# Optimization experiments

Hardware: AMD Instinct MI355X
Metric: run time of the kernel (lower is better)

Reference implementation:

```python
import jax, jax.numpy as jnp
import numpy as np

RC = 5.0
P = 6
N_ATOM = 4
N_AXIS = 8
EPS = 1e-5
C_RES = 0.89442719  # sqrt(0.8)
C_NEW = 0.4472      # ~sqrt(0.2)
BESSEL_PREF = float(np.sqrt(2.0 / RC))


def poly_cutoff(x):
    # nequip-style PolynomialCutoff, p=6
    xr = x / RC
    p = float(P)
    out = (1.0
           - (p + 1.0) * (p + 2.0) / 2.0 * xr ** P
           + p * (p + 2.0) * xr ** (P + 1)
           - p * (p + 1.0) / 2.0 * xr ** (P + 2))
    return jnp.where(xr < 1.0, out, 0.0)


def bessel(x, w):
    # x: [E], w: [n_basis] (trainable n*pi weights)
    return BESSEL_PREF * jnp.sin(w * x[:, None] / RC) / x[:, None]


def layer_norm(x, g, b):
    m = jnp.mean(x, axis=-1, keepdims=True)
    v = jnp.var(x, axis=-1, keepdims=True)
    return (x - m) * jax.lax.rsqrt(v + EPS) * g + b


def mlp3(x, W1, b1, W2, b2, W3, b3):
    # FFN: hidden block (linear-tanh-linear) + tanh + final linear
    h = jnp.tanh(x @ W1 + b1)
    h = jnp.tanh(h @ W2 + b2)
    return h @ W3 + b3


def resnet3(x, W1, b1, W2, b2, W3, b3):
    # ResNet: residual added where in/out dims match (final 64->64 linear)
    h = jnp.tanh(x @ W1 + b1)
    h = h @ W2 + b2
    return jnp.tanh(h) @ W3 + b3 + h


def seg_mean(x, idx, n):
    s = jax.ops.segment_sum(x, idx, num_segments=n)
    c = jax.ops.segment_sum(jnp.ones((x.shape[0],), x.dtype), idx, num_segments=n)
    c = jnp.maximum(c, 1.0).reshape((n,) + (1,) * (x.ndim - 1))
    return s / c


def setup_inputs() -> dict:
    key = jax.random.key(0)
    ks = iter(jax.random.split(key, 64))
    N, E, E2 = 40000, 320000, 160000
    NB, NR, NS, NA = 16, 64, 16, 8
    D = NA * NS  # 128 = n_hidden
    L = 2
    f32 = jnp.float32

    def nrm(shape, s=0.05):
        return jax.random.normal(next(ks), shape, dtype=f32) * s

    inp = {}
    inp['atom_types'] = jax.random.randint(next(ks), (N,), 0, N_ATOM, dtype=jnp.int32)
    ev = jax.random.normal(next(ks), (E, 3), dtype=f32)
    inp['env_vectors'] = ev
    inp['env_length'] = jnp.linalg.norm(ev, axis=-1) + 0.1
    inp['edge_length'] = jax.random.uniform(next(ks), (E2,), dtype=f32) * 4.0 + 0.5
    inp['env_index'] = jax.random.randint(next(ks), (2, E), 0, N, dtype=jnp.int32)
    inp['edge_index'] = jax.random.randint(next(ks), (2, E2), 0, N, dtype=jnp.int32)
    inp['bessel_w'] = jnp.arange(1, NB + 1, dtype=f32) * jnp.pi
    A = 2 * N_ATOM + NB  # 24
    inp['sr_W1'], inp['sr_b1'] = nrm((A, 64)), nrm((64,))
    inp['sr_W2'], inp['sr_b2'] = nrm((64, 64)), nrm((64,))
    inp['sr_W3'], inp['sr_b3'] = nrm((64, NS)), nrm((NS,))
    inp['rd_W1'], inp['rd_b1'] = nrm((A, 64)), nrm((64,))
    inp['rd_W2'], inp['rd_b2'] = nrm((64, 64)), nrm((64,))
    inp['rd_W3'], inp['rd_b3'] = nrm((64, NR)), nrm((NR,))
    inp['ne_emb_W'], inp['ne_emb_b'] = nrm((NR, D)), nrm((D,))
    inp['ne_nln_g'], inp['ne_nln_b'] = jnp.ones((D,), f32), jnp.zeros((D,), f32)
    inp['ne_eln_g'], inp['ne_eln_b'] = jnp.ones((NR,), f32), jnp.zeros((NR,), f32)
    inp['ly_emb_W'], inp['ly_emb_b'] = nrm((L, NR, D)), nrm((L, D))
    inp['ly_hid_W1'], inp['ly_hid_b1'] = nrm((L, 2 * D, 128)), nrm((L, 128))
    inp['ly_hid_W2'], inp['ly_hid_b2'] = nrm((L, 128, 128)), nrm((L, 128))
    inp['ly_hid_W3'], inp['ly_hid_b3'] = nrm((L, 128, D)), nrm((L, D))
    inp['ly_rdl_W1'], inp['ly_rdl_b1'] = nrm((L, NR + D, 64)), nrm((L, 64))
    inp['ly_rdl_W2'], inp['ly_rdl_b2'] = nrm((L, 64, 64)), nrm((L, 64))
    inp['ly_rdl_W3'], inp['ly_rdl_b3'] = nrm((L, 64, NR)), nrm((L, NR))
    inp['ly_nln_g'], inp['ly_nln_b'] = jnp.ones((L, D), f32), jnp.zeros((L, D), f32)
    inp['ly_eln_g'], inp['ly_eln_b'] = jnp.ones((L, NR), f32), jnp.zeros((L, NR), f32)
    return inp


def reference(atom_types, env_vectors, env_length, edge_length, env_index, edge_index,
              bessel_w,
              sr_W1, sr_b1, sr_W2, sr_b2, sr_W3, sr_b3,
              rd_W1, rd_b1, rd_W2, rd_b2, rd_W3, rd_b3,
              ne_emb_W, ne_emb_b, ne_nln_g, ne_nln_b, ne_eln_g, ne_eln_b,
              ly_emb_W, ly_emb_b,
              ly_hid_W1, ly_hid_b1, ly_hid_W2, ly_hid_b2, ly_hid_W3, ly_hid_b3,
              ly_rdl_W1, ly_rdl_b1, ly_rdl_W2, ly_rdl_b2, ly_rdl_W3, ly_rdl_b3,
              ly_nln_g, ly_nln_b, ly_eln_g, ly_eln_b):
    N = atom_types.shape[0]
    oh = jax.nn.one_hot(atom_types, N_ATOM, dtype=env_vectors.dtype)
    # atom_attr[index].transpose(1,0).reshape(E,-1) == concat of the two endpoints' one-hots
    env_attr = jnp.concatenate([oh[env_index[0]], oh[env_index[1]]], -1)   # [E, 2*n_atom]
    edge_attr = jnp.concatenate([oh[edge_index[0]], oh[edge_index[1]]], -1)
    ud_env = poly_cutoff(env_length)[:, None]    # [E, 1]
    ud_edge = poly_cutoff(edge_length)[:, None]  # [E2, 1]
    feat_env = jnp.concatenate([env_attr, ud_env * bessel(env_length, bessel_w)], -1)
    feat_edge = jnp.concatenate([edge_attr, ud_edge * bessel(edge_length, bessel_w)], -1)
    env_sqrt = mlp3(feat_env, sr_W1, sr_b1, sr_W2, sr_b2, sr_W3, sr_b3) * ud_env  # [E, n_sqrt]
    env_radial = layer_norm(mlp3(feat_env, rd_W1, rd_b1, rd_W2, rd_b2, rd_W3, rd_b3), ne_eln_g, ne_eln_b) * ud_env
    edge_radial = layer_norm(mlp3(feat_edge, rd_W1, rd_b1, rd_W2, rd_b2, rd_W3, rd_b3), ne_eln_g, ne_eln_b) * ud_edge
    # SE(2) aggregation: msg = [env_sqrt | ud * env_vectors]; outer product per node
    msg = env_sqrt[:, :, None] * (ud_env * env_vectors)[:, None, :]  # [E, n_sqrt, 3]
    agg = seg_mean(msg, env_index[1], N)                             # [N, n_sqrt, 3]
    gram = jnp.einsum('nds,nes->nde', agg, agg)[:, :, :N_AXIS]       # [N, n_sqrt, n_axis]
    node_emb = layer_norm(gram.reshape(N, -1), ne_nln_g, ne_nln_b)   # [N, D]
    env_hidden = (env_radial @ ne_emb_W + ne_emb_b) * (node_emb[env_index[1]] + node_emb[env_index[0]]) * 0.5
    edge_hidden = (edge_radial @ ne_emb_W + ne_emb_b) * (node_emb[edge_index[1]] + node_emb[edge_index[0]]) * 0.5
    for l in range(ly_emb_W.shape[0]):
        env_weight = env_radial @ ly_emb_W[l] + ly_emb_b[l]  # [E, D]
        agg2 = seg_mean(env_weight * node_emb[env_index[1]], env_index[1], N)
        node_emb = C_RES * node_emb + C_NEW * layer_norm(agg2, ly_nln_g[l], ly_nln_b[l])
        env_hidden = mlp3(jnp.concatenate([node_emb[env_index[0]], env_hidden], -1),
                          ly_hid_W1[l], ly_hid_b1[l], ly_hid_W2[l], ly_hid_b2[l], ly_hid_W3[l], ly_hid_b3[l])
        edge_hidden = mlp3(jnp.concatenate([node_emb[edge_index[0]], edge_hidden], -1),
                           ly_hid_W1[l], ly_hid_b1[l], ly_hid_W2[l], ly_hid_b2[l], ly_hid_W3[l], ly_hid_b3[l])
        env_radial = C_RES * env_radial + C_NEW * ud_env * layer_norm(
            resnet3(jnp.concatenate([env_radial, env_hidden], -1),
                    ly_rdl_W1[l], ly_rdl_b1[l], ly_rdl_W2[l], ly_rdl_b2[l], ly_rdl_W3[l], ly_rdl_b3[l]),
            ly_eln_g[l], ly_eln_b[l])
        edge_radial = C_RES * edge_radial + C_NEW * ud_edge * layer_norm(
            resnet3(jnp.concatenate([edge_radial, edge_hidden], -1),
                    ly_rdl_W1[l], ly_rdl_b1[l], ly_rdl_W2[l], ly_rdl_b2[l], ly_rdl_W3[l], ly_rdl_b3[l]),
            ly_eln_g[l], ly_eln_b[l])
    return env_radial, edge_radial, node_emb, env_hidden, edge_hidden
```

## Files before the change

### kernel.cpp

```cpp
#include <hip/hip_runtime.h>
#include <math.h>

#define C_RES 0.89442719f
#define C_NEW 0.4472f
#define LN_EPS 1e-5f
#define BESSEL_PREF 0.6324555320336759f
#define RC_INV 0.2f

typedef __attribute__((ext_vector_type(8))) short short8;
typedef __attribute__((ext_vector_type(8))) unsigned short u16x8;
typedef __attribute__((ext_vector_type(16))) float f32x16;

__device__ __forceinline__ float fast_tanh(float x) {
  float ax = fabsf(x);
  float e = __expf(2.0f * ax);
  float t = 1.0f - 2.0f / (e + 1.0f);
  return copysignf(t, x);
}

__device__ __forceinline__ unsigned short f2b(float f) {
  unsigned int u = __float_as_uint(f);
  unsigned int r = (u + 0x7FFFu + ((u >> 16) & 1u)) >> 16;
  return (unsigned short)r;
}

__device__ __forceinline__ u16x8 cvt8(const float* s) {
  const float4 v0 = *(const float4*)s;
  const float4 v1 = *(const float4*)(s + 4);
  u16x8 w;
  w[0]=f2b(v0.x); w[1]=f2b(v0.y); w[2]=f2b(v0.z); w[3]=f2b(v0.w);
  w[4]=f2b(v1.x); w[5]=f2b(v1.y); w[6]=f2b(v1.z); w[7]=f2b(v1.w);
  return w;
}

__device__ __forceinline__ float poly_cutoff(float x) {
  float xr = x * RC_INV;
  if (xr >= 1.0f) return 0.0f;
  float x2 = xr * xr;
  float x3 = x2 * xr;
  float x6 = x3 * x3;
  return 1.0f - 28.0f * x6 + 48.0f * x6 * xr - 21.0f * x6 * x2;
}

__device__ __forceinline__ int swz(int s, int kc) {
  return s ^ ((s >> 5) << 1) ^ ((kc & 1) << 2);
}

__global__ void zero_int_kernel(int* __restrict__ p, int n) {
  int i = blockIdx.x * blockDim.x + threadIdx.x;
  int stride = gridDim.x * blockDim.x;
  for (; i < n; i += stride) p[i] = 0;
}


__global__ void hist_kernel(int E, const int* __restrict__ idx, int* __restrict__ ecnt) {
  int t = blockIdx.x * 256 + threadIdx.x;
  if (t < E) atomicAdd(&ecnt[idx[E + t]], 1);
}

__launch_bounds__(1024)
__global__ void scan_kernel(const int* __restrict__ ecnt, int* __restrict__ eoff,
                            int* __restrict__ ecur, int n) {
  __shared__ int wsum[16];
  __shared__ int carry;
  const int tid = threadIdx.x;
  const int lane = tid & 63, wid = tid >> 6;
  if (tid == 0) carry = 0;
  __syncthreads();
  for (int b0 = 0; b0 < n; b0 += 1024) {
    const int i = b0 + tid;
    const int v = (i < n) ? ecnt[i] : 0;
    int incl = v;
    #pragma unroll
    for (int o = 1; o < 64; o <<= 1) {
      const int t = __shfl_up(incl, o);
      if (lane >= o) incl += t;
    }
    if (lane == 63) wsum[wid] = incl;
    __syncthreads();
    if (wid == 0) {
      const int wv = (lane < 16) ? wsum[lane] : 0;
      int wsc = wv;
      #pragma unroll
      for (int o = 1; o < 16; o <<= 1) {
        const int t = __shfl_up(wsc, o);
        if (lane >= o) wsc += t;
      }
      if (lane < 16) wsum[lane] = wsc - wv;
    }
    __syncthreads();
    const int c0 = carry;
    const int excl = c0 + wsum[wid] + incl - v;
    if (i < n) { eoff[i] = excl; ecur[i] = excl; }
    __syncthreads();
    if (tid == 1023) carry = c0 + wsum[15] + incl;
    __syncthreads();
  }
  if (tid == 0) eoff[n] = carry;
}

__global__ void scatter_kernel(int E, const int* __restrict__ idx,
                               int* __restrict__ ecur, int* __restrict__ perm) {
  int t = blockIdx.x * 256 + threadIdx.x;
  if (t < E) {
    const int pos = atomicAdd(&ecur[idx[E + t]], 1);
    perm[pos] = t;
  }
}

__global__ void pack_hid_weights(const float* __restrict__ W1,
                                 const float* __restrict__ W2,
                                 const float* __restrict__ W3,
                                 unsigned short* __restrict__ out)
{
  int t = blockIdx.x * 256 + threadIdx.x;
  if (t >= 131072) return;
  int l = t >> 16;
  int oidx = t & 65535;
  const float* src;
  int midx;
  if (oidx < 32768)      { src = W1 + l * 32768; midx = oidx; }
  else if (oidx < 49152) { src = W2 + l * 16384; midx = oidx - 32768; }
  else                   { src = W3 + l * 16384; midx = oidx - 49152; }
  int j = midx & 7;
  int lane = (midx >> 3) & 63;
  int blk = midx >> 9;
  int ct = blk & 3, kc = blk >> 2;
  int col = ct * 32 + (lane & 31);
  int k = kc * 16 + (lane >> 5) * 8 + j;
  out[l * 65536 + oidx] = f2b(src[k * 128 + col]);
}

__global__ void pack_rdl_weights(const float* __restrict__ W1,
                                 const float* __restrict__ W2,
                                 const float* __restrict__ W3,
                                 unsigned short* __restrict__ out)
{
  int t = blockIdx.x * 256 + threadIdx.x;
  if (t >= 40960) return;
  int l = t / 20480;
  int o = t - l * 20480;
  const float* src;
  int midx;
  if (o < 12288)      { src = W1 + l * 12288; midx = o; }
  else if (o < 16384) { src = W2 + l * 4096;  midx = o - 12288; }
  else                { src = W3 + l * 4096;  midx = o - 16384; }
  int j = midx & 7;
  int lane = (midx >> 3) & 63;
  int blk = midx >> 9;
  int ct = blk & 1, kc = blk >> 1;
  int col = ct * 32 + (lane & 31);
  int k = kc * 16 + (lane >> 5) * 8 + j;
  out[l * 20480 + o] = f2b(src[k * 64 + col]);
}

__global__ void pack_feat_weights(const float* __restrict__ rdW1,
                                  const float* __restrict__ rdW2,
                                  const float* __restrict__ rdW3,
                                  const float* __restrict__ srW1,
                                  const float* __restrict__ srW2,
                                  const float* __restrict__ srW3,
                                  unsigned short* __restrict__ out)
{
  int t = blockIdx.x * 256 + threadIdx.x;
  if (t >= 18432) return;
  const int blk = t >> 9, midx = t & 511;
  const int j = midx & 7, lane = (midx >> 3) & 63;
  const float* src; int kc, ct, K, NC;
  if (blk < 4)       { int b = blk;      src = rdW1; kc = b>>1; ct = b&1; K = 24; NC = 64; }
  else if (blk < 12) { int b = blk - 4;  src = rdW2; kc = b>>1; ct = b&1; K = 64; NC = 64; }
  else if (blk < 20) { int b = blk - 12; src = rdW3; kc = b>>1; ct = b&1; K = 64; NC = 64; }
  else if (blk < 24) { int b = blk - 20; src = srW1; kc = b>>1; ct = b&1; K = 24; NC = 64; }
  else if (blk < 32) { int b = blk - 24; src = srW2; kc = b>>1; ct = b&1; K = 64; NC = 64; }
  else               { int b = blk - 32; src = srW3; kc = b;    ct = 0;   K = 64; NC = 16; }
  const int col = ct * 32 + (lane & 31);
  const int k = kc * 16 + (lane >> 5) * 8 + j;
  const float v = (k < K && col < NC) ? src[k * NC + col] : 0.0f;
  out[t] = f2b(v);
}

__global__ void pack_emb_weights(const float* __restrict__ W,
                                 unsigned short* __restrict__ out)
{
  int t = blockIdx.x * 256 + threadIdx.x;
// ... 288 lines not shown
  float acc = 0.0f;
  for (int j = s; j < e; ++j) {
    const int ed = perm[j];
    acc += radial[(size_t)ed * 64 + lane];
  }
  const float inv = 1.0f / fmaxf((float)(e - s), 1.0f);
  mean_r[(size_t)w * 64 + lane] = acc * inv;
}


__launch_bounds__(256)
__global__ void node_update_gemm(
    int N, const float* __restrict__ mean_r, const int* __restrict__ ecnt,
    const float* __restrict__ W, const float* __restrict__ bias,
    const float* __restrict__ g, const float* __restrict__ b,
    float* __restrict__ node_emb)
{
  __shared__ __align__(16) float lw[64*128];
  __shared__ float lm[32][65];
  const int tid = threadIdx.x;
  const int base = blockIdx.x * 32;

  for (int i = tid; i < 8192; i += 256) lw[i] = W[i];
  {
    const int rr0 = tid >> 6, k = tid & 63;
    for (int rr = rr0; rr < 32; rr += 4) {
      const int n = base + rr;
      lm[rr][k] = (n < N) ? mean_r[(size_t)n*64 + k] : 0.0f;
    }
  }
  __syncthreads();

  const int r0 = (tid >> 5) * 4, j0 = (tid & 31) * 4;
  float acc[4][4];
  #pragma unroll
  for (int j = 0; j < 4; ++j) {
    const float bj = bias[j0 + j];
    acc[0][j] = bj; acc[1][j] = bj; acc[2][j] = bj; acc[3][j] = bj;
  }
  for (int k = 0; k < 64; ++k) {
    const float4 w = *(const float4*)&lw[k*128 + j0];
    const float s0 = lm[r0][k],   s1 = lm[r0+1][k];
    const float s2 = lm[r0+2][k], s3 = lm[r0+3][k];
    acc[0][0] += s0*w.x; acc[0][1] += s0*w.y; acc[0][2] += s0*w.z; acc[0][3] += s0*w.w;
    acc[1][0] += s1*w.x; acc[1][1] += s1*w.y; acc[1][2] += s1*w.z; acc[1][3] += s1*w.w;
    acc[2][0] += s2*w.x; acc[2][1] += s2*w.y; acc[2][2] += s2*w.z; acc[2][3] += s2*w.w;
    acc[3][0] += s3*w.x; acc[3][1] += s3*w.y; acc[3][2] += s3*w.z; acc[3][3] += s3*w.w;
  }

  const float g0 = g[j0], g1 = g[j0+1], g2 = g[j0+2], g3 = g[j0+3];
  const float bb0 = b[j0], bb1 = b[j0+1], bb2 = b[j0+2], bb3 = b[j0+3];
  #pragma unroll
  for (int i = 0; i < 4; ++i) {
    const int n = base + r0 + i;
    if (n >= N) continue;
    const float mask = (ecnt[n] > 0) ? 1.0f : 0.0f;
    const float4 old = *(const float4*)&node_emb[(size_t)n*128 + j0];
    const float x0 = old.x * acc[i][0] * mask;
    const float x1 = old.y * acc[i][1] * mask;
    const float x2 = old.z * acc[i][2] * mask;
    const float x3 = old.w * acc[i][3] * mask;
    float s = x0 + x1 + x2 + x3;
    float ss = x0*x0 + x1*x1 + x2*x2 + x3*x3;
    #pragma unroll
    for (int o = 1; o <= 16; o <<= 1) {
      s  += __shfl_xor(s, o);
      ss += __shfl_xor(ss, o);
    }
    const float m = s * (1.0f/128.0f);
    const float inv = rsqrtf(ss * (1.0f/128.0f) - m*m + LN_EPS);
    float4 o4;
    o4.x = C_RES*old.x + C_NEW*((x0 - m)*inv*g0 + bb0);
    o4.y = C_RES*old.y + C_NEW*((x1 - m)*inv*g1 + bb1);
    o4.z = C_RES*old.z + C_NEW*((x2 - m)*inv*g2 + bb2);
    o4.w = C_RES*old.w + C_NEW*((x3 - m)*inv*g3 + bb3);
    *(float4*)&node_emb[(size_t)n*128 + j0] = o4;
  }
}


__launch_bounds__(192)
__global__ void emb_mfma(
    int nrows,
    const float* __restrict__ radial,
    const unsigned short* __restrict__ wpck, const float* __restrict__ bias,
    const int* __restrict__ idx,
    const float* __restrict__ node_emb,
    float* __restrict__ out)
{
  __shared__ __align__(16) unsigned short afrag[12*512];
  __shared__ __align__(16) unsigned short wlds[16*512];
  __shared__ int i0l[96], i1l[96];

  const int tid = threadIdx.x, lane = tid & 63, wave = tid >> 6;
  const int base = blockIdx.x * 96, cl = lane & 31;

  for (int i = tid; i < 1024; i += 192)
    *(u16x8*)&wlds[i*8] = *(const u16x8*)&wpck[i*8];

  {
    const int r = tid >> 1, h = tid & 1;
    int rowg = base + r;
    if (rowg >= nrows) rowg = nrows - 1;
    if (h == 0) { i0l[r] = idx[rowg]; i1l[r] = idx[nrows + rowg]; }
    const float* rsrc = radial + (size_t)rowg * 64;
    #pragma unroll
    for (int g = 0; g < 4; ++g) {
      const int k = h*32 + g*8;
      const u16x8 w = cvt8(rsrc + k);
      const int kc = k >> 4;
      const int s_ = (r & 31) + 32*((k >> 3) & 1);
      *(u16x8*)&afrag[(kc*3 + (r>>5))*512 + swz(s_, kc)*8] = w;
    }
  }
  __syncthreads();

  f32x16 acc0, acc1, acc2, acc3;
  {
    const float bv0 = bias[cl], bv1 = bias[32+cl];
    const float bv2 = bias[64+cl], bv3 = bias[96+cl];
    #pragma unroll
    for (int q = 0; q < 16; ++q) { acc0[q]=bv0; acc1[q]=bv1; acc2[q]=bv2; acc3[q]=bv3; }
  }
  #pragma unroll
  for (int kc = 0; kc < 4; ++kc) {
    const short8 a  = *(const short8*)&afrag[(kc*3 + wave)*512 + swz(lane, kc)*8];
    const short8 w0 = *(const short8*)&wlds[(kc*4 + 0)*512 + lane*8];
    const short8 w1 = *(const short8*)&wlds[(kc*4 + 1)*512 + lane*8];
    const short8 w2 = *(const short8*)&wlds[(kc*4 + 2)*512 + lane*8];
    const short8 w3 = *(const short8*)&wlds[(kc*4 + 3)*512 + lane*8];
    acc0 = __builtin_amdgcn_mfma_f32_32x32x16_bf16(a, w0, acc0, 0, 0, 0);
    acc1 = __builtin_amdgcn_mfma_f32_32x32x16_bf16(a, w1, acc1, 0, 0, 0);
    acc2 = __builtin_amdgcn_mfma_f32_32x32x16_bf16(a, w2, acc2, 0, 0, 0);
    acc3 = __builtin_amdgcn_mfma_f32_32x32x16_bf16(a, w3, acc3, 0, 0, 0);
  }

  #pragma unroll
  for (int q = 0; q < 16; ++q) {
    const int row32 = (q & 3) + 8*(q >> 2) + 4*(lane >> 5);
    const int rloc  = wave*32 + row32;
    const int row   = base + rloc;
    if (row >= nrows) continue;
    const float* n0 = node_emb + (size_t)i0l[rloc]*128;
    const float* n1 = node_emb + (size_t)i1l[rloc]*128;
    float* op = out + (size_t)row*128;
    op[cl]    = acc0[q] * 0.5f * (n0[cl]    + n1[cl]);
    op[32+cl] = acc1[q] * 0.5f * (n0[32+cl] + n1[32+cl]);
    op[64+cl] = acc2[q] * 0.5f * (n0[64+cl] + n1[64+cl]);
    op[96+cl] = acc3[q] * 0.5f * (n0[96+cl] + n1[96+cl]);
  }
}


__launch_bounds__(256)
__global__ void hidrdl_mfma(
    int nrows, const int* __restrict__ idx0,
    const float* __restrict__ node_emb,
    const float* __restrict__ ud,
    const unsigned short* __restrict__ wpackh,
    const float* __restrict__ hb1, const float* __restrict__ hb2,
    const float* __restrict__ hb3,
    const unsigned short* __restrict__ wpackr,
    const float* __restrict__ rb1, const float* __restrict__ rb2,
    const float* __restrict__ rb3,
    const float* __restrict__ eln_g, const float* __restrict__ eln_b,
    float* __restrict__ hidden,
    float* __restrict__ radial)
{
  __shared__ __align__(16) unsigned short afragH[16384];
  __shared__ __align__(16) unsigned short afragR[8192];
  __shared__ __align__(16) unsigned short xg[4096];
  __shared__ __align__(16) unsigned short wg[4096];
  __shared__ float udl[128];

  const int tid  = threadIdx.x;
  const int lane = tid & 63;
  const int wave = tid >> 6;
  const int base = blockIdx.x * 128;
  const int cl   = lane & 31;

  const int r = tid >> 1, h2 = tid & 1;
  int rowg = base + r;
  if (rowg >= nrows) rowg = nrows - 1;
  const int rt0 = r >> 5;
  {
    const float* hsrc = hidden + (size_t)rowg * 128;
    const float* rsrc = radial + (size_t)rowg * 64;
    if (h2 == 0) udl[r] = ud[rowg];
    #pragma unroll
    for (int g = 0; g < 4; ++g) {
      const int k = h2*64 + g*16;
      #pragma unroll
      for (int gg = 0; gg < 2; ++gg) {
        const int kk = k + gg*8;
        const u16x8 w = cvt8(hsrc + kk);
        const int h = kk >> 4;
        const int s_ = (r & 31) + 32*((kk >> 3) & 1);
        *(u16x8*)&afragH[(rt0*8 + h)*512 + swz(s_, h)*8] = w;
      }
    }
    #pragma unroll
    for (int g = 0; g < 4; ++g) {
      const int k = h2*32 + g*8;
      const u16x8 w = cvt8(rsrc + k);
      const int kc = k >> 4;
      const int s_ = (r & 31) + 32*((k >> 3) & 1);
      *(u16x8*)&afragR[(rt0*4 + kc)*512 + swz(s_, kc)*8] = w;
    }
  }
  const float* xsrc0 = node_emb + (size_t)idx0[rowg] * 128;

  f32x16 acc[4];

  #pragma unroll
  for (int ct = 0; ct < 4; ++ct) {
    const float bv = hb1[ct*32 + cl];
    #pragma unroll
    for (int q = 0; q < 16; ++q) acc[ct][q] = bv;
  }
  for (int p = 0; p < 8; ++p) {
    __syncthreads();
    if (p < 4) {
      #pragma unroll
      for (int oo = 0; oo < 2; ++oo) {
        const int o = h2*2 + oo;
        const int k = p*32 + o*8;
        const u16x8 w = cvt8(xsrc0 + k);
        const int kc = p*2 + (o >> 1);
        const int s_ = (r & 31) + 32*(o & 1);
        *(u16x8*)&xg[ (rt0*2 + (o>>1))*512 + swz(s_, kc)*8 ] = w;
      }
    }
    #pragma unroll
    for (int i = 0; i < 2; ++i) {
      const int c = tid + i*256;
      *(u16x8*)&wg[c*8] = *(const u16x8*)&wpackh[p*4096 + c*8];
    }
    __syncthreads();
    #pragma unroll
    for (int kcl = 0; kcl < 2; ++kcl) {
      const int kc = p*2 + kcl;
      const short8 a = (p < 4)
        ? *(const short8*)&xg[ (wave*2 + kcl)*512 + swz(lane, kc)*8 ]
        : *(const short8*)&afragH[ (wave*8 + (kc-8))*512 + swz(lane, kc-8)*8 ];
      #pragma unroll
      for (int ct = 0; ct < 4; ++ct) {
        const short8 b = *(const short8*)&wg[ (kcl*4 + ct)*512 + lane*8 ];
        acc[ct] = __builtin_amdgcn_mfma_f32_32x32x16_bf16(a, b, acc[ct], 0, 0, 0);
      }
    }
  }

  #pragma unroll
  for (int ct = 0; ct < 4; ++ct) {
    const int kc  = ct*2 + ((lane >> 4) & 1);
    const int oct = (lane >> 3) & 1;
    const int j   = lane & 7;
    const int xk  = (oct << 1) ^ ((kc & 1) << 2);
    const int hi  = 4*(lane >> 5);
    const int bi  = (wave*8 + kc)*512 + oct*256 + j;
    #pragma unroll
    for (int q = 0; q < 16; ++q) {
      const int m32 = (q & 3) + 8*(q >> 2) + hi;
      afragH[bi + (m32 ^ xk)*8] = f2b(fast_tanh(acc[ct][q]));
    }
  }

  #pragma unroll
  for (int ct = 0; ct < 4; ++ct) {
    const float bv = hb2[ct*32 + cl];
    #pragma unroll
    for (int q = 0; q < 16; ++q) acc[ct][q] = bv;
  }
  for (int p = 0; p < 4; ++p) {
    __syncthreads();
    #pragma unroll
    for (int i = 0; i < 2; ++i) {
      const int c = tid + i*256;
      *(u16x8*)&wg[c*8] = *(const u16x8*)&wpackh[32768 + p*4096 + c*8];
    }
    __syncthreads();
    #pragma unroll
    for (int kcl = 0; kcl < 2; ++kcl) {
      const int kc = p*2 + kcl;
      const short8 a = *(const short8*)&afragH[ (wave*8 + kc)*512 + swz(lane, kc)*8 ];
      #pragma unroll
      for (int ct = 0; ct < 4; ++ct) {
        const short8 b = *(const short8*)&wg[ (kcl*4 + ct)*512 + lane*8 ];
        acc[ct] = __builtin_amdgcn_mfma_f32_32x32x16_bf16(a, b, acc[ct], 0, 0, 0);
      }
    }
  }

  #pragma unroll
  for (int ct = 0; ct < 4; ++ct) {
    const int kc  = ct*2 + ((lane >> 4) & 1);
    const int oct = (lane >> 3) & 1;
    const int j   = lane & 7;
    const int xk  = (oct << 1) ^ ((kc & 1) << 2);
    const int hi  = 4*(lane >> 5);
    const int bi  = (wave*8 + kc)*512 + oct*256 + j;
    #pragma unroll
    for (int q = 0; q < 16; ++q) {
      const int m32 = (q & 3) + 8*(q >> 2) + hi;
      afragH[bi + (m32 ^ xk)*8] = f2b(fast_tanh(acc[ct][q]));
    }
  }

  #pragma unroll
  for (int ct = 0; ct < 4; ++ct) {
    const float bv = hb3[ct*32 + cl];
    #pragma unroll
    for (int q = 0; q < 16; ++q) acc[ct][q] = bv;
  }
  for (int p = 0; p < 4; ++p) {
    __syncthreads();
    #pragma unroll
    for (int i = 0; i < 2; ++i) {
      const int c = tid + i*256;
      *(u16x8*)&wg[c*8] = *(const u16x8*)&wpackh[49152 + p*4096 + c*8];
    }
    __syncthreads();
    #pragma unroll
    for (int kcl = 0; kcl < 2; ++kcl) {
      const int kc = p*2 + kcl;
      const short8 a = *(const short8*)&afragH[ (wave*8 + kc)*512 + swz(lane, kc)*8 ];
      #pragma unroll
      for (int ct = 0; ct < 4; ++ct) {
        const short8 b = *(const short8*)&wg[ (kcl*4 + ct)*512 + lane*8 ];
        acc[ct] = __builtin_amdgcn_mfma_f32_32x32x16_bf16(a, b, acc[ct], 0, 0, 0);
      }
    }
  }

  #pragma unroll
  for (int ct = 0; ct < 4; ++ct) {
    const int col = ct*32 + cl;
    #pragma unroll
    for (int q = 0; q < 16; ++q) {
      const int row = base + wave*32 + (q & 3) + 8*(q >> 2) + 4*(lane >> 5);
      if (row < nrows) hidden[(size_t)row*128 + col] = acc[ct][q];
    }
  }
  #pragma unroll
  for (int ct = 0; ct < 4; ++ct) {
    const int kc  = ct*2 + ((lane >> 4) & 1);
    const int oct = (lane >> 3) & 1;
    const int j   = lane & 7;
    const int xk  = (oct << 1) ^ ((kc & 1) << 2);
    const int hi  = 4*(lane >> 5);
    const int bi  = (wave*8 + kc)*512 + oct*256 + j;
    #pragma unroll
    for (int q = 0; q < 16; ++q) {
      const int m32 = (q & 3) + 8*(q >> 2) + hi;
      afragH[bi + (m32 ^ xk)*8] = f2b(acc[ct][q]);
    }
  }

  f32x16 racc0, racc1;
  {
    const float bv0 = rb1[cl], bv1 = rb1[32 + cl];
    #pragma unroll
    for (int q = 0; q < 16; ++q) { racc0[q] = bv0; racc1[q] = bv1; }
  }
  for (int t = 0; t < 3; ++t) {
    __syncthreads();
    #pragma unroll
    for (int i = 0; i < 2; ++i) {
      const int c = tid + i*256;
      *(u16x8*)&wg[c*8] = *(const u16x8*)&wpackr[t*4096 + c*8];
    }
    __syncthreads();
    #pragma unroll
    for (int kk = 0; kk < 4; ++kk) {
      const int kc = t*4 + kk;
      const short8 a = (kc < 4)
        ? *(const short8*)&afragR[ (wave*4 + kc)*512 + swz(lane, kc)*8 ]
        : *(const short8*)&afragH[ (wave*8 + (kc-4))*512 + swz(lane, kc-4)*8 ];
      const short8 w0 = *(const short8*)&wg[ (kk*2 + 0)*512 + lane*8 ];
      const short8 w1 = *(const short8*)&wg[ (kk*2 + 1)*512 + lane*8 ];
      racc0 = __builtin_amdgcn_mfma_f32_32x32x16_bf16(a, w0, racc0, 0, 0, 0);
      racc1 = __builtin_amdgcn_mfma_f32_32x32x16_bf16(a, w1, racc1, 0, 0, 0);
    }
  }

  #pragma unroll
  for (int ct = 0; ct < 2; ++ct) {
    const int colh = ct*32 + cl;
    const int kc2  = colh >> 4;
    const int b3_  = (colh >> 3) & 1;
    const int jj   = colh & 7;
    const int blk  = (wave*8 + kc2)*512;
    #pragma unroll
    for (int q = 0; q < 16; ++q) {
      const int row32 = (q & 3) + 8*(q >> 2) + 4*(lane >> 5);
      const int s_ = (row32 & 31) + 32*b3_;
      const float v = ct ? racc1[q] : racc0[q];
      afragH[blk + swz(s_, kc2)*8 + jj] = f2b(fast_tanh(v));
    }
  }

  f32x16 rh0, rh1;
  {
    const float bv0 = rb2[cl], bv1 = rb2[32 + cl];
    #pragma unroll
    for (int q = 0; q < 16; ++q) { rh0[q] = bv0; rh1[q] = bv1; }
  }
  __syncthreads();
  #pragma unroll
  for (int i = 0; i < 2; ++i) {
    const int c = tid + i*256;
    *(u16x8*)&wg[c*8] = *(const u16x8*)&wpackr[24*512 + c*8];
  }
  __syncthreads();
  #pragma unroll
  for (int kc = 0; kc < 4; ++kc) {
    const short8 a  = *(const short8*)&afragH[ (wave*8 + kc)*512 + swz(lane, kc)*8 ];
    const short8 w0 = *(const short8*)&wg[ (kc*2 + 0)*512 + lane*8 ];
    const short8 w1 = *(const short8*)&wg[ (kc*2 + 1)*512 + lane*8 ];
    rh0 = __builtin_amdgcn_mfma_f32_32x32x16_bf16(a, w0, rh0, 0, 0, 0);
    rh1 = __builtin_amdgcn_mfma_f32_32x32x16_bf16(a, w1, rh1, 0, 0, 0);
  }

  #pragma unroll
  for (int ct = 0; ct < 2; ++ct) {
    const int colh = ct*32 + cl;
    const int kc2  = colh >> 4;
    const int b3_  = (colh >> 3) & 1;
    const int jj   = colh & 7;
    const int blk  = (wave*8 + 4 + kc2)*512;
    #pragma unroll
    for (int q = 0; q < 16; ++q) {
      const int row32 = (q & 3) + 8*(q >> 2) + 4*(lane >> 5);
      const int s_ = (row32 & 31) + 32*b3_;
      const float v = ct ? rh1[q] : rh0[q];
      afragH[blk + swz(s_, kc2)*8 + jj] = f2b(fast_tanh(v));
    }
  }

  {
    const float bv0 = rb3[cl], bv1 = rb3[32 + cl];
    #pragma unroll
    for (int q = 0; q < 16; ++q) { racc0[q] = bv0; racc1[q] = bv1; }
  }
  __syncthreads();
  #pragma unroll
  for (int i = 0; i < 2; ++i) {
    const int c = tid + i*256;
    *(u16x8*)&wg[c*8] = *(const u16x8*)&wpackr[32*512 + c*8];
  }
  __syncthreads();
  #pragma unroll
  for (int kc = 0; kc < 4; ++kc) {
    const short8 a  = *(const short8*)&afragH[ (wave*8 + 4 + kc)*512 + swz(lane, kc)*8 ];
    const short8 w0 = *(const short8*)&wg[ (kc*2 + 0)*512 + lane*8 ];
    const short8 w1 = *(const short8*)&wg[ (kc*2 + 1)*512 + lane*8 ];
    racc0 = __builtin_amdgcn_mfma_f32_32x32x16_bf16(a, w0, racc0, 0, 0, 0);
    racc1 = __builtin_amdgcn_mfma_f32_32x32x16_bf16(a, w1, racc1, 0, 0, 0);
  }

  const float eg0 = eln_g[cl],      eb0 = eln_b[cl];
  const float eg1 = eln_g[32 + cl], eb1 = eln_b[32 + cl];
  const int kcA = cl >> 4;
  const int kcB = (32 + cl) >> 4;
  const int jA  = cl & 7;
  const int bA  = (wave*4 + kcA)*512;
  const int bB  = (wave*4 + kcB)*512;
  const int b3A = (cl >> 3) & 1;
  const int b3B = ((32 + cl) >> 3) & 1;

  #pragma unroll
  for (int q = 0; q < 16; ++q) {
    const float v0 = racc0[q] + rh0[q];
    const float v1 = racc1[q] + rh1[q];
    float s = v0 + v1, ss = v0*v0 + v1*v1;
    #pragma unroll
    for (int o = 1; o <= 16; o <<= 1) {
      s  += __shfl_xor(s, o);
      ss += __shfl_xor(ss, o);
    }
    const float m   = s * (1.0f/64.0f);
    const float inv = rsqrtf(ss * (1.0f/64.0f) - m*m + LN_EPS);
    const int row32 = (q & 3) + 8*(q >> 2) + 4*(lane >> 5);
    const int rloc  = wave*32 + row32;
    const int row   = base + rloc;
    if (row < nrows) {
      const float u = udl[rloc];
      const int sA = (row32 & 31) + 32*b3A;
      const int sB = (row32 & 31) + 32*b3B;
      const float oldA = __uint_as_float((unsigned)afragR[bA + swz(sA, kcA)*8 + jA] << 16);
      const float oldB = __uint_as_float((unsigned)afragR[bB + swz(sB, kcB)*8 + jA] << 16);
      radial[(size_t)row*64 + cl]      = C_RES*oldA + C_NEW*u*((v0 - m)*inv*eg0 + eb0);
      radial[(size_t)row*64 + 32 + cl] = C_RES*oldB + C_NEW*u*((v1 - m)*inv*eg1 + eb1);
    }
  }
}


extern "C" void kernel_launch(void* const* d_in, const int* in_sizes, int n_in,
                              void* d_out, int out_size, void* d_ws, size_t ws_size,
                              hipStream_t stream)
{
  const int*   atom_types = (const int*)  d_in[0];
  const float* env_vec    = (const float*)d_in[1];
  const float* env_len    = (const float*)d_in[2];
  const float* edge_len   = (const float*)d_in[3];
  const int*   env_idx    = (const int*)  d_in[4];
  const int*   edge_idx   = (const int*)  d_in[5];
  const float* bessel_w   = (const float*)d_in[6];
  const float* srW1 = (const float*)d_in[7];  const float* srb1 = (const float*)d_in[8];
  const float* srW2 = (const float*)d_in[9];  const float* srb2 = (const float*)d_in[10];
  const float* srW3 = (const float*)d_in[11]; const float* srb3 = (const float*)d_in[12];
  const float* rdW1 = (const float*)d_in[13]; const float* rdb1 = (const float*)d_in[14];
  const float* rdW2 = (const float*)d_in[15]; const float* rdb2 = (const float*)d_in[16];
  const float* rdW3 = (const float*)d_in[17]; const float* rdb3 = (const float*)d_in[18];
  const float* ne_emb_W = (const float*)d_in[19]; const float* ne_emb_b = (const float*)d_in[20];
  const float* ne_nln_g = (const float*)d_in[21]; const float* ne_nln_b = (const float*)d_in[22];
  const float* ne_eln_g = (const float*)d_in[23]; const float* ne_eln_b = (const float*)d_in[24];
  const float* ly_emb_W = (const float*)d_in[25]; const float* ly_emb_b = (const float*)d_in[26];
  const float* ly_hid_W1 = (const float*)d_in[27]; const float* ly_hid_b1 = (const float*)d_in[28];
  const float* ly_hid_W2 = (const float*)d_in[29]; const float* ly_hid_b2 = (const float*)d_in[30];
  const float* ly_hid_W3 = (const float*)d_in[31]; const float* ly_hid_b3 = (const float*)d_in[32];
  const float* ly_rdl_W1 = (const float*)d_in[33]; const float* ly_rdl_b1 = (const float*)d_in[34];
  const float* ly_rdl_W2 = (const float*)d_in[35]; const float* ly_rdl_b2 = (const float*)d_in[36];
  const float* ly_rdl_W3 = (const float*)d_in[37]; const float* ly_rdl_b3 = (const float*)d_in[38];
  const float* ly_nln_g = (const float*)d_in[39]; const float* ly_nln_b = (const float*)d_in[40];
  const float* ly_eln_g = (const float*)d_in[41]; const float* ly_eln_b = (const float*)d_in[42];

  const int N  = in_sizes[0];
  const int E  = in_sizes[2];
  const int E2 = in_sizes[3];

  float* out = (float*)d_out;
  float* env_radial  = out;
  float* edge_radial = env_radial + (size_t)E * 64;
  float* node_emb    = edge_radial + (size_t)E2 * 64;
  float* env_hidden  = node_emb + (size_t)N * 128;
  float* edge_hidden = env_hidden + (size_t)E * 128;

  float* ws = (float*)d_ws;
  float* ud_env  = ws;  ws += E;
  float* ud_edge = ws;  ws += E2;
  float* aggS    = ws;  ws += (size_t)N * 48;
  float* msgbuf  = ws;  ws += (size_t)E * 20;
  float* mean_r  = msgbuf;
  unsigned short* wpack  = (unsigned short*)ws; ws += 65536;
  unsigned short* wpack2 = (unsigned short*)ws; ws += 20480;
  unsigned short* wpack3 = (unsigned short*)ws; ws += 9216;
  unsigned short* wpackE = (unsigned short*)ws; ws += 4096;
  int* ecnt = (int*)ws; ws += N;
  int* eoff = (int*)ws; ws += N + 1;
  int* ecur = (int*)ws; ws += N + 1;
  int* perm = (int*)ws; ws += E;

  const int gEr  = (E  + 95) / 96;
  const int gE2r = (E2 + 95) / 96;
  const int gEf  = (E  + 127) / 128;
  const int gE2f = (E2 + 127) / 128;
  const int gN32 = (N + 31) / 32;
  const int gN4w = (N * 64 + 255) / 256;

  zero_int_kernel<<<256, 256, 0, stream>>>(ecnt, N);
  hist_kernel<<<(E + 255) / 256, 256, 0, stream>>>(E, env_idx, ecnt);
  scan_kernel<<<1, 1024, 0, stream>>>(ecnt, eoff, ecur, N);
  scatter_kernel<<<(E + 255) / 256, 256, 0, stream>>>(E, env_idx, ecur, perm);

  pack_hid_weights<<<512, 256, 0, stream>>>(ly_hid_W1, ly_hid_W2, ly_hid_W3, wpack);
  pack_rdl_weights<<<160, 256, 0, stream>>>(ly_rdl_W1, ly_rdl_W2, ly_rdl_W3, wpack2);
  pack_feat_weights<<<72, 256, 0, stream>>>(rdW1, rdW2, rdW3, srW1, srW2, srW3, wpack3);
  pack_emb_weights<<<32, 256, 0, stream>>>(ne_emb_W, wpackE);

  feat_mfma<1><<<gEr, 192, 0, stream>>>(E, atom_types, env_len, env_vec, env_idx, bessel_w,
      wpack3, srb1, srb2, srb3, rdb1, rdb2, rdb3,
      ne_eln_g, ne_eln_b, env_radial, ud_env, msgbuf);
  feat_mfma<0><<<gE2r, 192, 0, stream>>>(E2, atom_types, edge_len, nullptr, edge_idx, bessel_w,
      wpack3, srb1, srb2, srb3, rdb1, rdb2, rdb3,
      ne_eln_g, ne_eln_b, edge_radial, ud_edge, nullptr);

  msg_gather_kernel<<<gN4w, 256, 0, stream>>>(N, eoff, perm, msgbuf, aggS);
  node_emb_kernel<<<N, 128, 0, stream>>>(N, aggS, ecnt, ne_nln_g, ne_nln_b, node_emb);

  emb_mfma<<<gEr, 192, 0, stream>>>(E, env_radial, wpackE, ne_emb_b, env_idx, node_emb, env_hidden);
  emb_mfma<<<gE2r, 192, 0, stream>>>(E2, edge_radial, wpackE, ne_emb_b, edge_idx, node_emb, edge_hidden);

  for (int l = 0; l < 2; ++l) {
    agg_gather_kernel<<<gN4w, 256, 0, stream>>>(N, eoff, perm, env_radial, mean_r);
    node_update_gemm<<<gN32, 256, 0, stream>>>(N, mean_r, ecnt,
        ly_emb_W + (size_t)l*64*128, ly_emb_b + (size_t)l*128,
        ly_nln_g + (size_t)l*128, ly_nln_b + (size_t)l*128, node_emb);

    hidrdl_mfma<<<gEf, 256, 0, stream>>>(E, env_idx, node_emb, ud_env,
        wpack + (size_t)l*65536,
        ly_hid_b1 + (size_t)l*128, ly_hid_b2 + (size_t)l*128, ly_hid_b3 + (size_t)l*128,
        wpack2 + (size_t)l*20480,
        ly_rdl_b1 + (size_t)l*64, ly_rdl_b2 + (size_t)l*64, ly_rdl_b3 + (size_t)l*64,
        ly_eln_g + (size_t)l*64, ly_eln_b + (size_t)l*64,
        env_hidden, env_radial);
    hidrdl_mfma<<<gE2f, 256, 0, stream>>>(E2, edge_idx, node_emb, ud_edge,
        wpack + (size_t)l*65536,
        ly_hid_b1 + (size_t)l*128, ly_hid_b2 + (size_t)l*128, ly_hid_b3 + (size_t)l*128,
        wpack2 + (size_t)l*20480,
        ly_rdl_b1 + (size_t)l*64, ly_rdl_b2 + (size_t)l*64, ly_rdl_b3 + (size_t)l*64,
        ly_eln_g + (size_t)l*64, ly_eln_b + (size_t)l*64,
        edge_hidden, edge_radial);
  }
}
```

Baseline: 1.324 ms.

## Double-buffer weight staging and load A fragments directly into registers in hidrdl kernel

The fused hidden/radial MLP kernel now double-buffers the weight tiles in shared memory, so the next chunk is staged while the current chunk's MFMAs run. This halves the barriers per step. The node-embedding, hidden and radial A-operands are loaded straight from global memory into registers in MFMA fragment layout, which drops the afragR, xg and udl shared buffers and cuts LDS use. That allows a launch bound of 3 blocks per CU. The cost is higher register pressure (aN, aH and aR arrays) and global re-reads of radial and ud in the epilogue.

```diff
diff --git a/kernel.cpp b/kernel.cpp
--- a/kernel.cpp
+++ b/kernel.cpp
@@ -30,6 +30,15 @@
   u16x8 w;
   w[0]=f2b(v0.x); w[1]=f2b(v0.y); w[2]=f2b(v0.z); w[3]=f2b(v0.w);
   w[4]=f2b(v1.x); w[5]=f2b(v1.y); w[6]=f2b(v1.z); w[7]=f2b(v1.w);
+  return w;
+}
+
+__device__ __forceinline__ short8 cvt8s(const float* s) {
+  const float4 v0 = *(const float4*)s;
+  const float4 v1 = *(const float4*)(s + 4);
+  short8 w;
+  w[0]=(short)f2b(v0.x); w[1]=(short)f2b(v0.y); w[2]=(short)f2b(v0.z); w[3]=(short)f2b(v0.w);
+  w[4]=(short)f2b(v1.x); w[5]=(short)f2b(v1.y); w[6]=(short)f2b(v1.z); w[7]=(short)f2b(v1.w);
   return w;
 }
 
@@ -624,7 +633,15 @@
 }
 
 
-__launch_bounds__(256)
+#define STAGE_WG(SRC, OFFU16, B) do {                                           \
+    _Pragma("unroll")                                                           \
+    for (int i_ = 0; i_ < 2; ++i_) {                                            \
+      const int c_ = tid + i_*256;                                              \
+      *(u16x8*)&wg[B][c_*8] = *(const u16x8*)&(SRC)[(OFFU16) + c_*8];           \
+    }                                                                           \
+  } while (0)
+
+__launch_bounds__(256, 3)
 __global__ void hidrdl_mfma(
     int nrows, const int* __restrict__ idx0,
     const float* __restrict__ node_emb,
@@ -640,47 +657,27 @@
     float* __restrict__ radial)
 {
   __shared__ __align__(16) unsigned short afragH[16384];
-  __shared__ __align__(16) unsigned short afragR[8192];
-  __shared__ __align__(16) unsigned short xg[4096];
-  __shared__ __align__(16) unsigned short wg[4096];
-  __shared__ float udl[128];
+  __shared__ __align__(16) unsigned short wg[2][4096];
 
   const int tid  = threadIdx.x;
   const int lane = tid & 63;
   const int wave = tid >> 6;
   const int base = blockIdx.x * 128;
   const int cl   = lane & 31;
-
-  const int r = tid >> 1, h2 = tid & 1;
-  int rowg = base + r;
-  if (rowg >= nrows) rowg = nrows - 1;
-  const int rt0 = r >> 5;
-  {
-    const float* hsrc = hidden + (size_t)rowg * 128;
-    const float* rsrc = radial + (size_t)rowg * 64;
-    if (h2 == 0) udl[r] = ud[rowg];
-    #pragma unroll
-    for (int g = 0; g < 4; ++g) {
-      const int k = h2*64 + g*16;
-      #pragma unroll
-      for (int gg = 0; gg < 2; ++gg) {
-        const int kk = k + gg*8;
-        const u16x8 w = cvt8(hsrc + kk);
-        const int h = kk >> 4;
-        const int s_ = (r & 31) + 32*((kk >> 3) & 1);
-        *(u16x8*)&afragH[(rt0*8 + h)*512 + swz(s_, h)*8] = w;
-      }
-    }
-    #pragma unroll
-    for (int g = 0; g < 4; ++g) {
-      const int k = h2*32 + g*8;
-      const u16x8 w = cvt8(rsrc + k);
-      const int kc = k >> 4;
-      const int s_ = (r & 31) + 32*((k >> 3) & 1);
-      *(u16x8*)&afragR[(rt0*4 + kc)*512 + swz(s_, kc)*8] = w;
-    }
-  }
-  const float* xsrc0 = node_emb + (size_t)idx0[rowg] * 128;
+  const int khalf = lane >> 5;
+
+  int lrow = base + wave*32 + cl;
+  if (lrow >= nrows) lrow = nrows - 1;
+  const int i0 = idx0[lrow];
+  const float* nsrc = node_emb + (size_t)i0 * 128;
+  const float* hsrc = hidden + (size_t)lrow * 128;
+  const float* rsrc = radial + (size_t)lrow * 64;
+
+  short8 aN[8], aH[8];
+  #pragma unroll
+  for (int kc = 0; kc < 8; ++kc) aN[kc] = cvt8s(nsrc + kc*16 + khalf*8);
+  #pragma unroll
+  for (int kc = 0; kc < 8; ++kc) aH[kc] = cvt8s(hsrc + kc*16 + khalf*8);
 
   f32x16 acc[4];
 
@@ -690,37 +687,23 @@
     #pragma unroll
     for (int q = 0; q < 16; ++q) acc[ct][q] = bv;
   }
+  STAGE_WG(wpackh, 0, 0);
+  __syncthreads();
+  #pragma unroll
   for (int p = 0; p < 8; ++p) {
-    __syncthreads();
-    if (p < 4) {
-      #pragma unroll
-      for (int oo = 0; oo < 2; ++oo) {
-        const int o = h2*2 + oo;
-        const int k = p*32 + o*8;
-        const u16x8 w = cvt8(xsrc0 + k);
-        const int kc = p*2 + (o >> 1);
-        const int s_ = (r & 31) + 32*(o & 1);
-        *(u16x8*)&xg[ (rt0*2 + (o>>1))*512 + swz(s_, kc)*8 ] = w;
-      }
-    }
-    #pragma unroll
-    for (int i = 0; i < 2; ++i) {
-      const int c = tid + i*256;
-      *(u16x8*)&wg[c*8] = *(const u16x8*)&wpackh[p*4096 + c*8];
-    }
-    __syncthreads();
+    if (p < 7) STAGE_WG(wpackh, (p+1)*4096, (p+1)&1);
+    else       STAGE_WG(wpackh, 32768, 0);
     #pragma unroll
     for (int kcl = 0; kcl < 2; ++kcl) {
       const int kc = p*2 + kcl;
-      const short8 a = (p < 4)
-        ? *(const short8*)&xg[ (wave*2 + kcl)*512 + swz(lane, kc)*8 ]
-        : *(const short8*)&afragH[ (wave*8 + (kc-8))*512 + swz(lane, kc-8)*8 ];
+      const short8 a = (kc < 8) ? aN[kc] : aH[kc-8];
       #pragma unroll
       for (int ct = 0; ct < 4; ++ct) {
-        const short8 b = *(const short8*)&wg[ (kcl*4 + ct)*512 + lane*8 ];
+        const short8 b = *(const short8*)&wg[p&1][ (kcl*4 + ct)*512 + lane*8 ];
         acc[ct] = __builtin_amdgcn_mfma_f32_32x32x16_bf16(a, b, acc[ct], 0, 0, 0);
       }
     }
+    __syncthreads();
   }
 
   #pragma unroll
@@ -744,24 +727,21 @@
     #pragma unroll
     for (int q = 0; q < 16; ++q) acc[ct][q] = bv;
   }
+  #pragma unroll
   for (int p = 0; p < 4; ++p) {
-    __syncthreads();
-    #pragma unroll
-    for (int i = 0; i < 2; ++i) {
-      const int c = tid + i*256;
-      *(u16x8*)&wg[c*8] = *(const u16x8*)&wpackh[32768 + p*4096 + c*8];
-    }
-    __syncthreads();
+    if (p < 3) STAGE_WG(wpackh, 32768 + (p+1)*4096, (p+1)&1);
+    else       STAGE_WG(wpackh, 49152, 0);
     #pragma unroll
     for (int kcl = 0; kcl < 2; ++kcl) {
       const int kc = p*2 + kcl;
       const short8 a = *(const short8*)&afragH[ (wave*8 + kc)*512 + swz(lane, kc)*8 ];
       #pragma unroll
       for (int ct = 0; ct < 4; ++ct) {
-        const short8 b = *(const short8*)&wg[ (kcl*4 + ct)*512 + lane*8 ];
+        const short8 b = *(const short8*)&wg[p&1][ (kcl*4 + ct)*512 + lane*8 ];
         acc[ct] = __builtin_amdgcn_mfma_f32_32x32x16_bf16(a, b, acc[ct], 0, 0, 0);
       }
     }
+    __syncthreads();
   }
 
   #pragma unroll
@@ -785,24 +765,21 @@
     #pragma unroll
     for (int q = 0; q < 16; ++q) acc[ct][q] = bv;
   }
+  #pragma unroll
   for (int p = 0; p < 4; ++p) {
-    __syncthreads();
-    #pragma unroll
-    for (int i = 0; i < 2; ++i) {
-      const int c = tid + i*256;
-      *(u16x8*)&wg[c*8] = *(const u16x8*)&wpackh[49152 + p*4096 + c*8];
-    }
-    __syncthreads();
+    if (p < 3) STAGE_WG(wpackh, 49152 + (p+1)*4096, (p+1)&1);
+    else       STAGE_WG(wpackr, 0, 0);
     #pragma unroll
     for (int kcl = 0; kcl < 2; ++kcl) {
       const int kc = p*2 + kcl;
       const short8 a = *(const short8*)&afragH[ (wave*8 + kc)*512 + swz(lane, kc)*8 ];
       #pragma unroll
       for (int ct = 0; ct < 4; ++ct) {
-        const short8 b = *(const short8*)&wg[ (kcl*4 + ct)*512 + lane*8 ];
+        const short8 b = *(const short8*)&wg[p&1][ (kcl*4 + ct)*512 + lane*8 ];
         acc[ct] = __builtin_amdgcn_mfma_f32_32x32x16_bf16(a, b, acc[ct], 0, 0, 0);
       }
     }
+    __syncthreads();
   }
 
   #pragma unroll
@@ -810,7 +787,7 @@
     const int col = ct*32 + cl;
     #pragma unroll
     for (int q = 0; q < 16; ++q) {
-      const int row = base + wave*32 + (q & 3) + 8*(q >> 2) + 4*(lane >> 5);
+      const int row = base + wave*32 + (q & 3) + 8*(q >> 2) + 4*khalf;
       if (row < nrows) hidden[(size_t)row*128 + col] = acc[ct][q];
     }
   }
@@ -829,31 +806,31 @@
     }
   }
 
+  short8 aR[4];
+  #pragma unroll
+  for (int kc = 0; kc < 4; ++kc) aR[kc] = cvt8s(rsrc + kc*16 + khalf*8);
+
   f32x16 racc0, racc1;
   {
     const float bv0 = rb1[cl], bv1 = rb1[32 + cl];
     #pragma unroll
     for (int q = 0; q < 16; ++q) { racc0[q] = bv0; racc1[q] = bv1; }
   }
+  #pragma unroll
   for (int t = 0; t < 3; ++t) {
-    __syncthreads();
-    #pragma unroll
-    for (int i = 0; i < 2; ++i) {
-      const int c = tid + i*256;
-      *(u16x8*)&wg[c*8] = *(const u16x8*)&wpackr[t*4096 + c*8];
-    }
-    __syncthreads();
+    if (t < 2) STAGE_WG(wpackr, (t+1)*4096, (t+1)&1);
+    else       STAGE_WG(wpackr, 12288, 1);
     #pragma unroll
     for (int kk = 0; kk < 4; ++kk) {
       const int kc = t*4 + kk;
-      const short8 a = (kc < 4)
-        ? *(const short8*)&afragR[ (wave*4 + kc)*512 + swz(lane, kc)*8 ]
+      const short8 a = (kc < 4) ? aR[kc]
         : *(const short8*)&afragH[ (wave*8 + (kc-4))*512 + swz(lane, kc-4)*8 ];
-      const short8 w0 = *(const short8*)&wg[ (kk*2 + 0)*512 + lane*8 ];
-      const short8 w1 = *(const short8*)&wg[ (kk*2 + 1)*512 + lane*8 ];
+      const short8 w0 = *(const short8*)&wg[t&1][ (kk*2 + 0)*512 + lane*8 ];
+      const short8 w1 = *(const short8*)&wg[t&1][ (kk*2 + 1)*512 + lane*8 ];
       racc0 = __builtin_amdgcn_mfma_f32_32x32x16_bf16(a, w0, racc0, 0, 0, 0);
       racc1 = __builtin_amdgcn_mfma_f32_32x32x16_bf16(a, w1, racc1, 0, 0, 0);
     }
+    __syncthreads();
   }
 
   #pragma unroll
@@ -865,7 +842,7 @@
     const int blk  = (wave*8 + kc2)*512;
     #pragma unroll
     for (int q = 0; q < 16; ++q) {
-      const int row32 = (q & 3) + 8*(q >> 2) + 4*(lane >> 5);
+      const int row32 = (q & 3) + 8*(q >> 2) + 4*khalf;
       const int s_ = (row32 & 31) + 32*b3_;
       const float v = ct ? racc1[q] : racc0[q];
       afragH[blk + swz(s_, kc2)*8 + jj] = f2b(fast_tanh(v));
@@ -878,21 +855,16 @@
     #pragma unroll
     for (int q = 0; q < 16; ++q) { rh0[q] = bv0; rh1[q] = bv1; }
   }
-  __syncthreads();
-  #pragma unroll
-  for (int i = 0; i < 2; ++i) {
-    const int c = tid + i*256;
-    *(u16x8*)&wg[c*8] = *(const u16x8*)&wpackr[24*512 + c*8];
-  }
-  __syncthreads();
+  STAGE_WG(wpackr, 16384, 0);
   #pragma unroll
   for (int kc = 0; kc < 4; ++kc) {
     const short8 a  = *(const short8*)&afragH[ (wave*8 + kc)*512 + swz(lane, kc)*8 ];
-    const short8 w0 = *(const short8*)&wg[ (kc*2 + 0)*512 + lane*8 ];
-    const short8 w1 = *(const short8*)&wg[ (kc*2 + 1)*512 + lane*8 ];
+    const short8 w0 = *(const short8*)&wg[1][ (kc*2 + 0)*512 + lane*8 ];
+    const short8 w1 = *(const short8*)&wg[1][ (kc*2 + 1)*512 + lane*8 ];
     rh0 = __builtin_amdgcn_mfma_f32_32x32x16_bf16(a, w0, rh0, 0, 0, 0);
     rh1 = __builtin_amdgcn_mfma_f32_32x32x16_bf16(a, w1, rh1, 0, 0, 0);
   }
+  __syncthreads();
 
   #pragma unroll
   for (int ct = 0; ct < 2; ++ct) {
@@ -903,7 +875,7 @@
     const int blk  = (wave*8 + 4 + kc2)*512;
     #pragma unroll
     for (int q = 0; q < 16; ++q) {
-      const int row32 = (q & 3) + 8*(q >> 2) + 4*(lane >> 5);
+      const int row32 = (q & 3) + 8*(q >> 2) + 4*khalf;
       const int s_ = (row32 & 31) + 32*b3_;
       const float v = ct ? rh1[q] : rh0[q];
       afragH[blk + swz(s_, kc2)*8 + jj] = f2b(fast_tanh(v));
@@ -915,31 +887,18 @@
     #pragma unroll
     for (int q = 0; q < 16; ++q) { racc0[q] = bv0; racc1[q] = bv1; }
   }
-  __syncthreads();
-  #pragma unroll
-  for (int i = 0; i < 2; ++i) {
-    const int c = tid + i*256;
-    *(u16x8*)&wg[c*8] = *(const u16x8*)&wpackr[32*512 + c*8];
-  }
-  __syncthreads();
   #pragma unroll
   for (int kc = 0; kc < 4; ++kc) {
     const short8 a  = *(const short8*)&afragH[ (wave*8 + 4 + kc)*512 + swz(lane, kc)*8 ];
-    const short8 w0 = *(const short8*)&wg[ (kc*2 + 0)*512 + lane*8 ];
-    const short8 w1 = *(const short8*)&wg[ (kc*2 + 1)*512 + lane*8 ];
+    const short8 w0 = *(const short8*)&wg[0][ (kc*2 + 0)*512 + lane*8 ];
+    const short8 w1 = *(const short8*)&wg[0][ (kc*2 + 1)*512 + lane*8 ];
     racc0 = __builtin_amdgcn_mfma_f32_32x32x16_bf16(a, w0, racc0, 0, 0, 0);
     racc1 = __builtin_amdgcn_mfma_f32_32x32x16_bf16(a, w1, racc1, 0, 0, 0);
   }
 
   const float eg0 = eln_g[cl],      eb0 = eln_b[cl];
   const float eg1 = eln_g[32 + cl], eb1 = eln_b[32 + cl];
-  const int kcA = cl >> 4;
-  const int kcB = (32 + cl) >> 4;
-  const int jA  = cl & 7;
-  const int bA  = (wave*4 + kcA)*512;
-  const int bB  = (wave*4 + kcB)*512;
-  const int b3A = (cl >> 3) & 1;
-  const int b3B = ((32 + cl) >> 3) & 1;
+  const float* rtile = radial + (size_t)(base + wave*32) * 64;
 
   #pragma unroll
   for (int q = 0; q < 16; ++q) {
@@ -953,15 +912,12 @@
     }
     const float m   = s * (1.0f/64.0f);
     const float inv = rsqrtf(ss * (1.0f/64.0f) - m*m + LN_EPS);
-    const int row32 = (q & 3) + 8*(q >> 2) + 4*(lane >> 5);
-    const int rloc  = wave*32 + row32;
-    const int row   = base + rloc;
+    const int row32 = (q & 3) + 8*(q >> 2) + 4*khalf;
+    const int row   = base + wave*32 + row32;
     if (row < nrows) {
-      const float u = udl[rloc];
-      const int sA = (row32 & 31) + 32*b3A;
-      const int sB = (row32 & 31) + 32*b3B;
-      const float oldA = __uint_as_float((unsigned)afragR[bA + swz(sA, kcA)*8 + jA] << 16);
-      const float oldB = __uint_as_float((unsigned)afragR[bB + swz(sB, kcB)*8 + jA] << 16);
+      const float u = ud[row];
+      const float oldA = rtile[row32*64 + cl];
+      const float oldB = rtile[row32*64 + 32 + cl];
       radial[(size_t)row*64 + cl]      = C_RES*oldA + C_NEW*u*((v0 - m)*inv*eg0 + eb0);
       radial[(size_t)row*64 + 32 + cl] = C_RES*oldB + C_NEW*u*((v1 - m)*inv*eg1 + eb1);
     }
```

After: 1.312 ms. Within noise of the previous version (-0.9%).
